# Optimization experiments

Measured on AMD Instinct MI355X. Metric: run time of the kernel, lower is better.

Reference implementation:

```python
import jax, jax.numpy as jnp
import numpy as np

NQ = 5  # 1 ancilla qubit (index 0) + 4 register qubits (indices 1..4)


def setup_inputs():
    key = jax.random.key(0)
    k1, k2 = jax.random.split(key)
    inputs = jax.random.uniform(k1, (32, 32, 32, 3), dtype=jnp.float32)
    kernel = jax.random.normal(k2, (8, 1, 15), dtype=jnp.float32) * 0.3
    return {"inputs": inputs, "kernel": kernel}


def _apply1(state, U, q):
    # state: [P, 2,2,2,2,2]; U: [2,2] or [P,2,2]; qubit q at axis q+1
    state = jnp.moveaxis(state, q + 1, -1)
    if U.ndim == 3:
        state = jnp.einsum('nij,n...j->n...i', U, state)
    else:
        state = jnp.einsum('ij,n...j->n...i', U, state)
    return jnp.moveaxis(state, -1, q + 1)


def _apply2(state, U, qa, qb):
    # U: [4,4] acting on (qa, qb)
    state = jnp.moveaxis(state, (qa + 1, qb + 1), (-2, -1))
    sh = state.shape
    state = state.reshape(sh[:-2] + (4,))
    state = jnp.einsum('ij,n...j->n...i', U, state)
    state = state.reshape(sh)
    return jnp.moveaxis(state, (-2, -1), (qa + 1, qb + 1))


def _rx_batch(theta):
    # cirq.rx(theta): [[cos(t/2), -i sin(t/2)], [-i sin(t/2), cos(t/2)]]; theta: [P]
    c = jnp.cos(theta / 2).astype(jnp.complex64)
    s = jnp.sin(theta / 2).astype(jnp.complex64)
    return jnp.stack([jnp.stack([c, -1j * s], -1), jnp.stack([-1j * s, c], -1)], -2)


def _cxpow(e):
    # CXPowGate(exponent=e): identity on control=0 block, X^e on control=1 block
    o = jnp.ones((), jnp.complex64)
    z = jnp.zeros((), jnp.complex64)
    lam = jnp.exp(1j * jnp.pi * e.astype(jnp.complex64))
    a = (o + lam) / 2
    b = (o - lam) / 2
    return jnp.stack([jnp.stack([o, z, z, z]), jnp.stack([z, o, z, z]),
                      jnp.stack([z, z, a, b]), jnp.stack([z, z, b, a])])


def _czpow(e):
    o = jnp.ones((), jnp.complex64)
    lam = jnp.exp(1j * jnp.pi * e.astype(jnp.complex64))
    return jnp.diag(jnp.stack([o, o, o, lam]))


def _simulate(angles, params):
    # angles: [P, 4*C] pixel values per patch; params: [5*C] learned exponents
    P = angles.shape[0]
    C = angles.shape[1] // 4
    state = jnp.zeros((P, 2 ** NQ), jnp.complex64).at[:, 0].set(1.0)
    state = state.reshape((P,) + (2,) * NQ)
    Hm = jnp.asarray(np.array([[1, 1], [1, -1]]) / np.sqrt(2), jnp.complex64)
    state = _apply1(state, Hm, 0)  # H on ancilla
    for j in range(C):
        # embed: rx(pi * pixel) on the 4 register qubits
        for i in range(4):
            state = _apply1(state, _rx_batch(jnp.pi * angles[:, 4 * j + i]), 1 + i)
        p = params[5 * j:5 * j + 5]
        # intra-register entanglement: CXPow with (control, target) pairs
        for g, (qc, qt) in enumerate(((1, 2), (2, 3), (3, 4), (4, 1))):
            state = _apply2(state, _cxpow(p[g]), qc, qt)
        # deposit: CZPow between register qubit 0 and the ancilla (symmetric)
        state = _apply2(state, _czpow(p[4]), 1, 0)
    # <X_0> = 2 Re sum conj(psi[0,rest]) psi[1,rest]
    exp = 2.0 * jnp.sum(jnp.real(jnp.conj(state[:, 0]) * state[:, 1]),
                        axis=tuple(range(1, NQ)))
    return exp.astype(jnp.float32)  # [P]


def reference(inputs, kernel):
    B, H, W, C = inputs.shape
    nx, ny = H - 1, W - 1
    # normalize_tensor_by_index: inputs already in [0,1] -> identity
    x = inputs
    # 2x2 stride-1 patches; last axis order (0,0),(0,1),(1,0),(1,1) row-major
    p = jnp.stack([x[:, :-1, :-1], x[:, :-1, 1:], x[:, 1:, :-1], x[:, 1:, 1:]], axis=-1)
    # [B,nx,ny,C,4] -> [B*nx*ny, C*4]: index 4*c + pixel (channel-major, matches transpose+reshape in call())
    angles = p.reshape(-1, C * 4)
    params = kernel[:, 0, :]  # [K, 5*C]
    exp = jax.vmap(lambda pr: _simulate(angles, pr))(params)  # [K, B*nx*ny]
    out = exp.reshape(params.shape[0], B, nx, ny).transpose(1, 2, 3, 0)  # [B,nx,ny,K]
    out = jnp.arccos(jnp.clip(out, -1 + 1e-5, 1 - 1e-5)) / jnp.pi
    return out  # activation=None -> linear
```

## Files before the change

### kernel.cpp

```cpp
#include <hip/hip_runtime.h>
#include <math.h>

#define PI_F 3.14159265358979323846f

template<int S>
__device__ __forceinline__ void apply_rx(float* sr, float* si, float c, float s) {
#pragma unroll
    for (int i = 0; i < 32; ++i) {
        if (i & S) continue;
        const int j = i + S;
        const float r0 = sr[i], m0 = si[i], r1 = sr[j], m1 = si[j];
        sr[i] = fmaf(c, r0,  s * m1);
        si[i] = fmaf(c, m0, -s * r1);
        sr[j] = fmaf(c, r1,  s * m0);
        si[j] = fmaf(c, m1, -s * r0);
    }
}

template<int Sc, int St>
__device__ __forceinline__ void apply_cxpow(float* sr, float* si, float e) {
    float sl, cl;
    sincosf(PI_F * e, &sl, &cl);
    const float ar = 0.5f * (1.0f + cl), ai =  0.5f * sl;
    const float br = 0.5f * (1.0f - cl), bi = -0.5f * sl;
#pragma unroll
    for (int i = 0; i < 32; ++i) {
        if (!(i & Sc) || (i & St)) continue;
        const int j = i + St;
        const float r0 = sr[i], m0 = si[i], r1 = sr[j], m1 = si[j];
        sr[i] = ar * r0 - ai * m0 + br * r1 - bi * m1;
        si[i] = ar * m0 + ai * r0 + br * m1 + bi * r1;
        sr[j] = br * r0 - bi * m0 + ar * r1 - ai * m1;
        si[j] = br * m0 + bi * r0 + ar * m1 + ai * r1;
    }
}

__device__ __forceinline__ void apply_czpow(float* sr, float* si, float e) {
    float sl, cl;
    sincosf(PI_F * e, &sl, &cl);
#pragma unroll
    for (int i = 0; i < 32; ++i) {
        if ((i & 24) != 24) continue;
        const float r = sr[i], m = si[i];
        sr[i] = r * cl - m * sl;
        si[i] = r * sl + m * cl;
    }
}

__global__ __launch_bounds__(256)
void u1_circuit_kernel(const float* __restrict__ inp,
                       const float* __restrict__ ker,
                       float* __restrict__ out,
                       int total) {
    const int t = blockIdx.x * blockDim.x + threadIdx.x;
    if (t >= total) return;

    const int r   = t & 7;
    const int pix = t >> 3;
    const int iy  = pix % 31;
    const int tq  = pix / 31;
    const int ix  = tq % 31;
    const int b   = tq / 31;

    const float* xp = inp + ((size_t)(b * 32 + ix) * 32 + iy) * 3;
    const float* pp = ker + r * 15;

    float sr[32], si[32];
#pragma unroll
    for (int i = 0; i < 32; ++i) { sr[i] = 0.0f; si[i] = 0.0f; }
    sr[0]  = 0.70710678118654752440f;
    sr[16] = 0.70710678118654752440f;

#pragma unroll
    for (int j = 0; j < 3; ++j) {
        const float a0 = xp[j];
        const float a1 = xp[3 + j];
        const float a2 = xp[96 + j];
        const float a3 = xp[99 + j];
        float c, s;
        sincosf(0.5f * PI_F * a0, &s, &c); apply_rx<8>(sr, si, c, s);
        sincosf(0.5f * PI_F * a1, &s, &c); apply_rx<4>(sr, si, c, s);
        sincosf(0.5f * PI_F * a2, &s, &c); apply_rx<2>(sr, si, c, s);
        sincosf(0.5f * PI_F * a3, &s, &c); apply_rx<1>(sr, si, c, s);

        const float* p = pp + 5 * j;
        apply_cxpow<8, 4>(sr, si, p[0]);
        apply_cxpow<4, 2>(sr, si, p[1]);
        apply_cxpow<2, 1>(sr, si, p[2]);
        apply_cxpow<1, 8>(sr, si, p[3]);
        apply_czpow(sr, si, p[4]);
    }

    float dot = 0.0f;
#pragma unroll
    for (int k = 0; k < 16; ++k)
        dot += sr[k] * sr[k + 16] + si[k] * si[k + 16];
    float e = 2.0f * dot;
    e = fminf(fmaxf(e, -1.0f + 1e-5f), 1.0f - 1e-5f);
    out[t] = acosf(e) * (1.0f / PI_F);
}

extern "C" void kernel_launch(void* const* d_in, const int* in_sizes, int n_in,
                              void* d_out, int out_size, void* d_ws, size_t ws_size,
                              hipStream_t stream) {
    const float* inp = (const float*)d_in[0];
    const float* ker = (const float*)d_in[1];
    float* out = (float*)d_out;
    const int total = out_size;
    const int block = 256;
    const int grid = (total + block - 1) / block;
    u1_circuit_kernel<<<grid, block, 0, stream>>>(inp, ker, out, total);
}
```

Before: 75.51 us.

## Split state by ancilla branch and analytically compute the first RX layer

The 32-amplitude state is split into two 16-amplitude branches, one per ancilla value. The CZ phase then acts only on one branch, and the final expectation becomes a dot product of the two branches. The first layer of RX gates on the zero state is written as a closed-form product state, and the CX-pow gates are rewritten as a single complex multiply of the amplitude difference. Precise sincosf calls are replaced with the hardware sin/cos builtins taking revolutions, which trades some accuracy for fewer instructions.

```diff
diff --git a/kernel.cpp b/kernel.cpp
--- a/kernel.cpp
+++ b/kernel.cpp
@@ -3,10 +3,11 @@
 
 #define PI_F 3.14159265358979323846f
 
+
 template<int S>
-__device__ __forceinline__ void apply_rx(float* sr, float* si, float c, float s) {
+__device__ __forceinline__ void rx16(float* sr, float* si, float c, float s) {
 #pragma unroll
-    for (int i = 0; i < 32; ++i) {
+    for (int i = 0; i < 16; ++i) {
         if (i & S) continue;
         const int j = i + S;
         const float r0 = sr[i], m0 = si[i], r1 = sr[j], m1 = si[j];
@@ -18,33 +19,35 @@
 }
 
 template<int Sc, int St>
-__device__ __forceinline__ void apply_cxpow(float* sr, float* si, float e) {
-    float sl, cl;
-    sincosf(PI_F * e, &sl, &cl);
-    const float ar = 0.5f * (1.0f + cl), ai =  0.5f * sl;
-    const float br = 0.5f * (1.0f - cl), bi = -0.5f * sl;
+__device__ __forceinline__ void cx16(float* sr, float* si, float br, float bi) {
 #pragma unroll
-    for (int i = 0; i < 32; ++i) {
+    for (int i = 0; i < 16; ++i) {
         if (!(i & Sc) || (i & St)) continue;
         const int j = i + St;
-        const float r0 = sr[i], m0 = si[i], r1 = sr[j], m1 = si[j];
-        sr[i] = ar * r0 - ai * m0 + br * r1 - bi * m1;
-        si[i] = ar * m0 + ai * r0 + br * m1 + bi * r1;
-        sr[j] = br * r0 - bi * m0 + ar * r1 - ai * m1;
-        si[j] = br * m0 + bi * r0 + ar * m1 + ai * r1;
+        const float dr = sr[j] - sr[i], di = si[j] - si[i];
+        const float ur = br * dr - bi * di;
+        const float ui = fmaf(br, di, bi * dr);
+        sr[i] += ur; si[i] += ui;
+        sr[j] -= ur; si[j] -= ui;
     }
 }
 
-__device__ __forceinline__ void apply_czpow(float* sr, float* si, float e) {
-    float sl, cl;
-    sincosf(PI_F * e, &sl, &cl);
+__device__ __forceinline__ void cz16(float* sr, float* si, float cl, float sl) {
 #pragma unroll
-    for (int i = 0; i < 32; ++i) {
-        if ((i & 24) != 24) continue;
-        const float r = sr[i], m = si[i];
-        sr[i] = r * cl - m * sl;
-        si[i] = r * sl + m * cl;
+    for (int m = 0; m < 16; ++m) {
+        if (!(m & 8)) continue;
+        const float r = sr[m], q = si[m];
+        sr[m] = r * cl - q * sl;
+        si[m] = fmaf(r, sl, q * cl);
     }
+}
+
+__device__ __forceinline__ void bcoef(float e, float& br, float& bi) {
+    const float rev = e * 0.5f;
+    const float sl = __builtin_amdgcn_sinf(rev);
+    const float cl = __builtin_amdgcn_cosf(rev);
+    br = 0.5f * (1.0f - cl);
+    bi = -0.5f * sl;
 }
 
 __global__ __launch_bounds__(256)
@@ -65,39 +68,82 @@
     const float* xp = inp + ((size_t)(b * 32 + ix) * 32 + iy) * 3;
     const float* pp = ker + r * 15;
 
-    float sr[32], si[32];
+    float c1, s1, c2, s2, c3, s3, c4, s4;
+    {
+        const float a0 = xp[0], a1 = xp[3], a2 = xp[96], a3 = xp[99];
+        s1 = __builtin_amdgcn_sinf(a0 * 0.25f); c1 = __builtin_amdgcn_cosf(a0 * 0.25f);
+        s2 = __builtin_amdgcn_sinf(a1 * 0.25f); c2 = __builtin_amdgcn_cosf(a1 * 0.25f);
+        s3 = __builtin_amdgcn_sinf(a2 * 0.25f); c3 = __builtin_amdgcn_cosf(a2 * 0.25f);
+        s4 = __builtin_amdgcn_sinf(a3 * 0.25f); c4 = __builtin_amdgcn_cosf(a3 * 0.25f);
+    }
+    float t2[4], t3[8], mg[16];
+    t2[0] = c1 * c2; t2[1] = c1 * s2; t2[2] = s1 * c2; t2[3] = s1 * s2;
 #pragma unroll
-    for (int i = 0; i < 32; ++i) { sr[i] = 0.0f; si[i] = 0.0f; }
-    sr[0]  = 0.70710678118654752440f;
-    sr[16] = 0.70710678118654752440f;
+    for (int x = 0; x < 8; ++x)  t3[x] = t2[x >> 1] * ((x & 1) ? s3 : c3);
+#pragma unroll
+    for (int x = 0; x < 16; ++x) mg[x] = t3[x >> 1] * ((x & 1) ? s4 : c4);
+
+    float p0r[16], p0i[16];
+#pragma unroll
+    for (int m = 0; m < 16; ++m) {
+        const int pc = __builtin_popcount(m) & 3;
+        p0r[m] = (pc == 0) ? mg[m] : ((pc == 2) ? -mg[m] : 0.0f);
+        p0i[m] = (pc == 1) ? -mg[m] : ((pc == 3) ? mg[m] : 0.0f);
+    }
+
+    float br, bi;
+    bcoef(pp[0], br, bi); cx16<8, 4>(p0r, p0i, br, bi);
+    bcoef(pp[1], br, bi); cx16<4, 2>(p0r, p0i, br, bi);
+    bcoef(pp[2], br, bi); cx16<2, 1>(p0r, p0i, br, bi);
+    bcoef(pp[3], br, bi); cx16<1, 8>(p0r, p0i, br, bi);
+
+    float p1r[16], p1i[16];
+    {
+        const float rev = pp[4] * 0.5f;
+        const float sl = __builtin_amdgcn_sinf(rev);
+        const float cl = __builtin_amdgcn_cosf(rev);
+#pragma unroll
+        for (int m = 0; m < 16; ++m) {
+            if (m & 8) {
+                p1r[m] = p0r[m] * cl - p0i[m] * sl;
+                p1i[m] = fmaf(p0r[m], sl, p0i[m] * cl);
+            } else {
+                p1r[m] = p0r[m];
+                p1i[m] = p0i[m];
+            }
+        }
+    }
 
 #pragma unroll
-    for (int j = 0; j < 3; ++j) {
-        const float a0 = xp[j];
-        const float a1 = xp[3 + j];
-        const float a2 = xp[96 + j];
-        const float a3 = xp[99 + j];
+    for (int j = 1; j < 3; ++j) {
+        const float a0 = xp[j], a1 = xp[3 + j], a2 = xp[96 + j], a3 = xp[99 + j];
         float c, s;
-        sincosf(0.5f * PI_F * a0, &s, &c); apply_rx<8>(sr, si, c, s);
-        sincosf(0.5f * PI_F * a1, &s, &c); apply_rx<4>(sr, si, c, s);
-        sincosf(0.5f * PI_F * a2, &s, &c); apply_rx<2>(sr, si, c, s);
-        sincosf(0.5f * PI_F * a3, &s, &c); apply_rx<1>(sr, si, c, s);
+        s = __builtin_amdgcn_sinf(a0 * 0.25f); c = __builtin_amdgcn_cosf(a0 * 0.25f);
+        rx16<8>(p0r, p0i, c, s); rx16<8>(p1r, p1i, c, s);
+        s = __builtin_amdgcn_sinf(a1 * 0.25f); c = __builtin_amdgcn_cosf(a1 * 0.25f);
+        rx16<4>(p0r, p0i, c, s); rx16<4>(p1r, p1i, c, s);
+        s = __builtin_amdgcn_sinf(a2 * 0.25f); c = __builtin_amdgcn_cosf(a2 * 0.25f);
+        rx16<2>(p0r, p0i, c, s); rx16<2>(p1r, p1i, c, s);
+        s = __builtin_amdgcn_sinf(a3 * 0.25f); c = __builtin_amdgcn_cosf(a3 * 0.25f);
+        rx16<1>(p0r, p0i, c, s); rx16<1>(p1r, p1i, c, s);
 
         const float* p = pp + 5 * j;
-        apply_cxpow<8, 4>(sr, si, p[0]);
-        apply_cxpow<4, 2>(sr, si, p[1]);
-        apply_cxpow<2, 1>(sr, si, p[2]);
-        apply_cxpow<1, 8>(sr, si, p[3]);
-        apply_czpow(sr, si, p[4]);
+        bcoef(p[0], br, bi); cx16<8, 4>(p0r, p0i, br, bi); cx16<8, 4>(p1r, p1i, br, bi);
+        bcoef(p[1], br, bi); cx16<4, 2>(p0r, p0i, br, bi); cx16<4, 2>(p1r, p1i, br, bi);
+        bcoef(p[2], br, bi); cx16<2, 1>(p0r, p0i, br, bi); cx16<2, 1>(p1r, p1i, br, bi);
+        bcoef(p[3], br, bi); cx16<1, 8>(p0r, p0i, br, bi); cx16<1, 8>(p1r, p1i, br, bi);
+
+        const float rev = p[4] * 0.5f;
+        cz16(p1r, p1i, __builtin_amdgcn_cosf(rev), __builtin_amdgcn_sinf(rev));
     }
 
     float dot = 0.0f;
 #pragma unroll
-    for (int k = 0; k < 16; ++k)
-        dot += sr[k] * sr[k + 16] + si[k] * si[k + 16];
-    float e = 2.0f * dot;
-    e = fminf(fmaxf(e, -1.0f + 1e-5f), 1.0f - 1e-5f);
-    out[t] = acosf(e) * (1.0f / PI_F);
+    for (int m = 0; m < 16; ++m)
+        dot = fmaf(p0r[m], p1r[m], fmaf(p0i[m], p1i[m], dot));
+
+    dot = fminf(fmaxf(dot, -1.0f + 1e-5f), 1.0f - 1e-5f);
+    out[t] = acosf(dot) * (1.0f / PI_F);
 }
 
 extern "C" void kernel_launch(void* const* d_in, const int* in_sizes, int n_in,
```

Measured after the change: 67.43 us. 1.12x faster.
